# Kernel tuning notes

Hardware: AMD Instinct MI355X
Metric: run time of the kernel (lower is better)

## Reference

```python
import jax, jax.numpy as jnp
import numpy as np

H = 1536          # hidden_size
NUM_HEADS = 12
NUM_KV = 2
HEAD_DIM = 128
GQA_REP = NUM_HEADS // NUM_KV  # 6
MAX_CACHE = 131072
SCALE = HEAD_DIM ** -0.5


def setup_inputs() -> dict:
    key = jax.random.key(0)
    ks = jax.random.split(key, 8)
    w = 0.02  # weight init scale for numerical sanity
    return {
        "hidden_states": jax.random.normal(ks[0], (1, H, 1, 1), dtype=jnp.float32),
        "Wq": jax.random.normal(ks[1], (NUM_HEADS * HEAD_DIM, H), dtype=jnp.float32) * w,
        "Wk": jax.random.normal(ks[2], (NUM_KV * HEAD_DIM, H), dtype=jnp.float32) * w,
        "Wv": jax.random.normal(ks[3], (NUM_KV * HEAD_DIM, H), dtype=jnp.float32) * w,
        "Wo": jax.random.normal(ks[4], (H, NUM_HEADS * HEAD_DIM), dtype=jnp.float32) * w,
        "kv_cache_k": jax.random.normal(ks[5], (1, NUM_KV, MAX_CACHE, HEAD_DIM), dtype=jnp.float32),
        "kv_cache_v": jax.random.normal(ks[6], (1, NUM_KV, MAX_CACHE, HEAD_DIM), dtype=jnp.float32),
        "pos": MAX_CACHE - 1,  # python int: current cache write position
    }


def reference(hidden_states, Wq, Wk, Wv, Wo, kv_cache_k, kv_cache_v, pos):
    # 1x1 Conv2d on a [1,H,1,1] tensor == matvec.
    x = hidden_states.reshape(H)                      # [H]
    q = (Wq @ x).reshape(NUM_KV, GQA_REP, HEAD_DIM)   # [g, r, d]
    k = (Wk @ x).reshape(NUM_KV, 1, HEAD_DIM)         # [g, 1, d]
    v = (Wv @ x).reshape(NUM_KV, 1, HEAD_DIM)
    # in-place cache write at pos (pos < MAX_CACHE in this setup)
    kc = jax.lax.dynamic_update_slice(kv_cache_k[0], k, (0, pos, 0))  # [g, L, d]
    vc = jax.lax.dynamic_update_slice(kv_cache_v[0], v, (0, pos, 0))
    seq_len = min(pos + 1, MAX_CACHE)  # pos is a python int -> static slice
    kc = kc[:, :seq_len, :]
    vc = vc[:, :seq_len, :]
    # GQA without materializing repeated K/V: fold repeat into the q head axis.
    scores = jnp.einsum('grd,gld->grl', q, kc) * SCALE       # [g, r, L]
    attn = jax.nn.softmax(scores, axis=-1)
    out = jnp.einsum('grl,gld->grd', attn, vc)               # [g, r, d]
    y = Wo @ out.reshape(NUM_HEADS * HEAD_DIM)               # [H]
    return y.reshape(1, H, 1, 1)
```

## Files before the change

### kernel.cpp

```cpp
#include <hip/hip_runtime.h>
#include <math.h>

#define HDIM 1536
#define NUM_HEADS 12
#define NUM_KV 2
#define HEAD_DIM 128
#define GQA_REP 6
#define MAX_CACHE 131072
#define SCALE 0.08838834764831845f

#define WS_Q    0
#define WS_OUT  2048
#define WS_L2   4096
#define WS_PART 65536
#define REC 132

#define UNITS_PER_G 1024
#define NEG_BIG (-1.0e30f)
#define MASK_NEG (-1.0e38f)

__global__ __launch_bounds__(256) void proj_qkv(
    const float* __restrict__ x, const float* __restrict__ Wq,
    const float* __restrict__ Wk, const float* __restrict__ Wv,
    float* __restrict__ kv_k, float* __restrict__ kv_v,
    const int* __restrict__ pos_p, float* __restrict__ ws)
{
    int r    = (blockIdx.x * 256 + threadIdx.x) >> 6;
    int lane = threadIdx.x & 63;

    const float* Wrow;
    if (r < HDIM)            Wrow = Wq + (size_t)r * HDIM;
    else if (r < HDIM + 256) Wrow = Wk + (size_t)(r - HDIM) * HDIM;
    else                     Wrow = Wv + (size_t)(r - HDIM - 256) * HDIM;

    const float4* w4 = (const float4*)Wrow;
    const float4* x4 = (const float4*)x;
    float sum = 0.f;
#pragma unroll
    for (int it = 0; it < 6; ++it) {
        float4 a = w4[lane + 64 * it];
        float4 b = x4[lane + 64 * it];
        sum += a.x * b.x + a.y * b.y + a.z * b.z + a.w * b.w;
    }
#pragma unroll
    for (int off = 32; off >= 1; off >>= 1) sum += __shfl_xor(sum, off);

    if (lane == 0) {
        if (r < HDIM) {
            ws[WS_Q + r] = sum * SCALE;
        } else {
            int pos = *pos_p;
            if (r < HDIM + 256) {
                int j = r - HDIM; int g = j >> 7, d = j & 127;
                kv_k[((size_t)g * MAX_CACHE + pos) * HEAD_DIM + d] = sum;
            } else {
                int j = r - HDIM - 256; int g = j >> 7, d = j & 127;
                kv_v[((size_t)g * MAX_CACHE + pos) * HEAD_DIM + d] = sum;
            }
        }
    }
}

__global__ __launch_bounds__(256) void attn_decode(
    const float* __restrict__ kv_k, const float* __restrict__ kv_v,
    const int* __restrict__ pos_p, float* __restrict__ ws)
{
    int wv   = (blockIdx.x * 256 + threadIdx.x) >> 6;
    int lane = threadIdx.x & 63;
    int g = wv >> 10;
    int u = wv & 1023;
    int h = lane >> 5;
    int j = lane & 31;

    int seq_len = *pos_p + 1;
    if (seq_len > MAX_CACHE) seq_len = MAX_CACHE;

    const float* qb = ws + WS_Q + g * (GQA_REP * HEAD_DIM);
    float4 q[GQA_REP];
#pragma unroll
    for (int r = 0; r < GQA_REP; ++r)
        q[r] = ((const float4*)(qb + r * HEAD_DIM))[j];

    float  m[GQA_REP], l[GQA_REP];
    float4 acc[GQA_REP];
#pragma unroll
    for (int r = 0; r < GQA_REP; ++r) {
        m[r] = NEG_BIG; l[r] = 0.f;
        acc[r].x = acc[r].y = acc[r].z = acc[r].w = 0.f;
    }

    int base = u * 128;
    const float4* Kb = (const float4*)(kv_k + ((size_t)g * MAX_CACHE + base) * HEAD_DIM);
    const float4* Vb = (const float4*)(kv_v + ((size_t)g * MAX_CACHE + base) * HEAD_DIM);
    int idx = h * 32 + j;

    float4 Kc = Kb[idx];
    float4 Vc = Vb[idx];

    for (int i = 0; i < 64; ++i) {
        float4 Kn, Vn;
        if (i < 63) {
            Kn = Kb[idx + (i + 1) * 64];
            Vn = Vb[idx + (i + 1) * 64];
        }
        int p = base + 2 * i + h;
        float maskadd = (p < seq_len) ? 0.f : MASK_NEG;

        float s[GQA_REP];
#pragma unroll
        for (int r = 0; r < GQA_REP; ++r) {
            float sr = Kc.x * q[r].x + Kc.y * q[r].y + Kc.z * q[r].z + Kc.w * q[r].w;
#pragma unroll
            for (int off = 16; off >= 1; off >>= 1) sr += __shfl_xor(sr, off);
            s[r] = sr + maskadd;
        }
#pragma unroll
        for (int r = 0; r < GQA_REP; ++r) {
            float mn    = fmaxf(m[r], s[r]);
            float alpha = __expf(m[r] - mn);
            float pw    = __expf(s[r] - mn);
            l[r] = l[r] * alpha + pw;
            acc[r].x = acc[r].x * alpha + pw * Vc.x;
            acc[r].y = acc[r].y * alpha + pw * Vc.y;
            acc[r].z = acc[r].z * alpha + pw * Vc.z;
            acc[r].w = acc[r].w * alpha + pw * Vc.w;
            m[r] = mn;
        }
        Kc = Kn; Vc = Vn;
    }

#pragma unroll
    for (int r = 0; r < GQA_REP; ++r) {
        float mo = __shfl_xor(m[r], 32);
        float lo = __shfl_xor(l[r], 32);
        float4 ao;
        ao.x = __shfl_xor(acc[r].x, 32);
        ao.y = __shfl_xor(acc[r].y, 32);
        ao.z = __shfl_xor(acc[r].z, 32);
        ao.w = __shfl_xor(acc[r].w, 32);
        float M  = fmaxf(m[r], mo);
        float a0 = __expf(m[r] - M);
        float a1 = __expf(mo   - M);
        float L  = l[r] * a0 + lo * a1;
        float4 A;
        A.x = acc[r].x * a0 + ao.x * a1;
        A.y = acc[r].y * a0 + ao.y * a1;
        A.z = acc[r].z * a0 + ao.z * a1;
        A.w = acc[r].w * a0 + ao.w * a1;

        float* rec = ws + WS_PART + ((size_t)(g * UNITS_PER_G + u) * GQA_REP + r) * REC;
        if (lane < 32) ((float4*)(rec + 4))[j] = A;
        if (lane == 0) { rec[0] = M; rec[1] = L; }
    }
}

__global__ __launch_bounds__(64) void combine1(float* __restrict__ ws)
{
    int b  = blockIdx.x;
    int hh = b >> 5;
    int s  = b & 31;
    int g = hh / GQA_REP, r = hh % GQA_REP;
    int t  = threadIdx.x;
    int um = t & 31;

    const float* base = ws + WS_PART +
        ((size_t)(g * UNITS_PER_G + s * 32) * GQA_REP + r) * REC;
    const float* rec = base + (size_t)um * GQA_REP * REC;
    float mu = rec[0], lu = rec[1];

    float M = mu;
#pragma unroll
    for (int off = 16; off >= 1; off >>= 1) M = fmaxf(M, __shfl_xor(M, off));
    float w = __expf(mu - M);
    float L = lu * w;
#pragma unroll
    for (int off = 16; off >= 1; off >>= 1) L += __shfl_xor(L, off);

    float2 a; a.x = 0.f; a.y = 0.f;
    for (int uu = 0; uu < 32; ++uu) {
        float wu = __shfl(w, uu);
        float2 av = ((const float2*)(base + (size_t)uu * GQA_REP * REC + 4))[t];
        a.x += wu * av.x;
        a.y += wu * av.y;
    }
    float* orec = ws + WS_L2 + (size_t)(hh * 32 + s) * REC;
    ((float2*)(orec + 4))[t] = a;
    if (t == 0) { orec[0] = M; orec[1] = L; }
}

__global__ __launch_bounds__(64) void combine2(float* __restrict__ ws)
{
    int hh = blockIdx.x;
    int t  = threadIdx.x;
    int um = t & 31;

    const float* base = ws + WS_L2 + (size_t)(hh * 32) * REC;
    const float* rec  = base + (size_t)um * REC;
    float mu = rec[0], lu = rec[1];

    float M = mu;
#pragma unroll
    for (int off = 16; off >= 1; off >>= 1) M = fmaxf(M, __shfl_xor(M, off));
    float w = __expf(mu - M);
    float L = lu * w;
#pragma unroll
    for (int off = 16; off >= 1; off >>= 1) L += __shfl_xor(L, off);

    float2 a; a.x = 0.f; a.y = 0.f;
    for (int uu = 0; uu < 32; ++uu) {
        float wu = __shfl(w, uu);
        float2 av = ((const float2*)(base + (size_t)uu * REC + 4))[t];
        a.x += wu * av.x;
        a.y += wu * av.y;
    }
    float invL = 1.f / L;
    ws[WS_OUT + hh * HEAD_DIM + 2 * t]     = a.x * invL;
    ws[WS_OUT + hh * HEAD_DIM + 2 * t + 1] = a.y * invL;
}

__global__ __launch_bounds__(256) void proj_out(
    const float* __restrict__ Wo, const float* __restrict__ ws,
    float* __restrict__ y)
{
    int r    = (blockIdx.x * 256 + threadIdx.x) >> 6;
    int lane = threadIdx.x & 63;
    const float4* w4 = (const float4*)(Wo + (size_t)r * HDIM);
    const float4* o4 = (const float4*)(ws + WS_OUT);
    float sum = 0.f;
#pragma unroll
    for (int it = 0; it < 6; ++it) {
        float4 a = w4[lane + 64 * it];
        float4 b = o4[lane + 64 * it];
        sum += a.x * b.x + a.y * b.y + a.z * b.z + a.w * b.w;
    }
#pragma unroll
    for (int off = 32; off >= 1; off >>= 1) sum += __shfl_xor(sum, off);
    if (lane == 0) y[r] = sum;
}

extern "C" void kernel_launch(void* const* d_in, const int* in_sizes, int n_in,
                              void* d_out, int out_size, void* d_ws, size_t ws_size,
                              hipStream_t stream) {
    const float* x   = (const float*)d_in[0];
    const float* Wq  = (const float*)d_in[1];
    const float* Wk  = (const float*)d_in[2];
    const float* Wv  = (const float*)d_in[3];
    const float* Wo  = (const float*)d_in[4];
    float*       kvk = (float*)d_in[5];
    float*       kvv = (float*)d_in[6];
    const int*   pos = (const int*)d_in[7];
    float* ws = (float*)d_ws;
    float* y  = (float*)d_out;

    proj_qkv   <<<512, 256, 0, stream>>>(x, Wq, Wk, Wv, kvk, kvv, pos, ws);
    attn_decode<<<512, 256, 0, stream>>>(kvk, kvv, pos, ws);
    combine1   <<<384,  64, 0, stream>>>(ws);
    combine2   <<< 12,  64, 0, stream>>>(ws);
    proj_out   <<<384, 256, 0, stream>>>(Wo, ws, y);
}
```

Before: 314.0 us.

## Split each attention unit across a block's four waves and merge partials in LDS

The attention kernel now assigns each 128-position unit to a whole 256-thread block, with each wave handling 32 positions, instead of one wave per unit. The grid grows from 512 to 2048 blocks. The four per-wave partial softmax states are merged in shared memory before one record per unit is written, so the combine kernels stay unchanged. The aim is more parallelism and memory-level concurrency on the bandwidth-bound KV scan, at the cost of an LDS merge, a block barrier and a shorter per-wave prefetch pipeline. A launch-bounds occupancy hint is also added.

```diff
diff --git a/kernel.cpp b/kernel.cpp
--- a/kernel.cpp
+++ b/kernel.cpp
@@ -61,16 +61,19 @@
     }
 }
 
-__global__ __launch_bounds__(256) void attn_decode(
+__global__ __launch_bounds__(256, 4) void attn_decode(
     const float* __restrict__ kv_k, const float* __restrict__ kv_v,
     const int* __restrict__ pos_p, float* __restrict__ ws)
 {
-    int wv   = (blockIdx.x * 256 + threadIdx.x) >> 6;
+    __shared__ float lds[4][GQA_REP][REC];
+
+    int b    = blockIdx.x;
+    int g    = b >> 10;
+    int ublk = b & 1023;
+    int wid  = threadIdx.x >> 6;
     int lane = threadIdx.x & 63;
-    int g = wv >> 10;
-    int u = wv & 1023;
-    int h = lane >> 5;
-    int j = lane & 31;
+    int h    = lane >> 5;
+    int j    = lane & 31;
 
     int seq_len = *pos_p + 1;
     if (seq_len > MAX_CACHE) seq_len = MAX_CACHE;
@@ -89,21 +92,21 @@
         acc[r].x = acc[r].y = acc[r].z = acc[r].w = 0.f;
     }
 
-    int base = u * 128;
-    const float4* Kb = (const float4*)(kv_k + ((size_t)g * MAX_CACHE + base) * HEAD_DIM);
-    const float4* Vb = (const float4*)(kv_v + ((size_t)g * MAX_CACHE + base) * HEAD_DIM);
+    int wbase = ublk * 128 + wid * 32;
+    const float4* Kb = (const float4*)(kv_k + ((size_t)g * MAX_CACHE + wbase) * HEAD_DIM);
+    const float4* Vb = (const float4*)(kv_v + ((size_t)g * MAX_CACHE + wbase) * HEAD_DIM);
     int idx = h * 32 + j;
 
     float4 Kc = Kb[idx];
     float4 Vc = Vb[idx];
 
-    for (int i = 0; i < 64; ++i) {
+    for (int i = 0; i < 16; ++i) {
         float4 Kn, Vn;
-        if (i < 63) {
+        if (i < 15) {
             Kn = Kb[idx + (i + 1) * 64];
             Vn = Vb[idx + (i + 1) * 64];
         }
-        int p = base + 2 * i + h;
+        int p = wbase + 2 * i + h;
         float maskadd = (p < seq_len) ? 0.f : MASK_NEG;
 
         float s[GQA_REP];
@@ -148,8 +151,30 @@
         A.z = acc[r].z * a0 + ao.z * a1;
         A.w = acc[r].w * a0 + ao.w * a1;
 
-        float* rec = ws + WS_PART + ((size_t)(g * UNITS_PER_G + u) * GQA_REP + r) * REC;
-        if (lane < 32) ((float4*)(rec + 4))[j] = A;
+        if (lane < 32) ((float4*)&lds[wid][r][4])[j] = A;
+        if (lane == 0) { lds[wid][r][0] = M; lds[wid][r][1] = L; }
+    }
+    __syncthreads();
+
+    for (int r = wid; r < GQA_REP; r += 4) {
+        float m0 = lds[0][r][0], m1 = lds[1][r][0];
+        float m2 = lds[2][r][0], m3 = lds[3][r][0];
+        float M = fmaxf(fmaxf(m0, m1), fmaxf(m2, m3));
+        float w0 = __expf(m0 - M), w1 = __expf(m1 - M);
+        float w2 = __expf(m2 - M), w3 = __expf(m3 - M);
+        float L = lds[0][r][1] * w0 + lds[1][r][1] * w1
+                + lds[2][r][1] * w2 + lds[3][r][1] * w3;
+
+        float2 a0v = ((const float2*)&lds[0][r][4])[lane];
+        float2 a1v = ((const float2*)&lds[1][r][4])[lane];
+        float2 a2v = ((const float2*)&lds[2][r][4])[lane];
+        float2 a3v = ((const float2*)&lds[3][r][4])[lane];
+        float2 a;
+        a.x = a0v.x * w0 + a1v.x * w1 + a2v.x * w2 + a3v.x * w3;
+        a.y = a0v.y * w0 + a1v.y * w1 + a2v.y * w2 + a3v.y * w3;
+
+        float* rec = ws + WS_PART + ((size_t)(g * UNITS_PER_G + ublk) * GQA_REP + r) * REC;
+        ((float2*)(rec + 4))[lane] = a;
         if (lane == 0) { rec[0] = M; rec[1] = L; }
     }
 }
@@ -252,9 +277,9 @@
     float* ws = (float*)d_ws;
     float* y  = (float*)d_out;
 
-    proj_qkv   <<<512, 256, 0, stream>>>(x, Wq, Wk, Wv, kvk, kvv, pos, ws);
-    attn_decode<<<512, 256, 0, stream>>>(kvk, kvv, pos, ws);
-    combine1   <<<384,  64, 0, stream>>>(ws);
-    combine2   <<< 12,  64, 0, stream>>>(ws);
-    proj_out   <<<384, 256, 0, stream>>>(Wo, ws, y);
-}
+    proj_qkv   <<<512,  256, 0, stream>>>(x, Wq, Wk, Wv, kvk, kvv, pos, ws);
+    attn_decode<<<2048, 256, 0, stream>>>(kvk, kvv, pos, ws);
+    combine1   <<<384,   64, 0, stream>>>(ws);
+    combine2   <<< 12,   64, 0, stream>>>(ws);
+    proj_out   <<<384,  256, 0, stream>>>(Wo, ws, y);
+}
```

New measurement: 315.8 us. Within noise of the previous version (+0.6%).
